# Kernel tuning notes

Measured on AMD Instinct MI355X. Metric: run time of the kernel, lower is better.

## Reference

```python
import jax, jax.numpy as jnp
import numpy as np

B, C, O, H, W = 8, 64, 64, 128, 128


def conv3x3(x, w, b):
    # x: [B,Cin,H,W], w: [Cout,Cin,3,3], stride 1, padding 1
    y = jax.lax.conv_general_dilated(
        x, w, window_strides=(1, 1), padding=((1, 1), (1, 1)),
        dimension_numbers=("NCHW", "OIHW", "NCHW"))
    return y + b[None, :, None, None]


def setup_inputs() -> dict:
    key = jax.random.key(0)
    ks = jax.random.split(key, 6)
    fan = C * 9
    x = jax.random.normal(ks[0], (B, C, H, W), dtype=jnp.float32)
    w_main = jax.random.normal(ks[1], (O, C, 3, 3), dtype=jnp.float32) / np.sqrt(fan)
    # small offset weights keep sampled locations near the regular grid (realistic post-training regime)
    w_offset = jax.random.normal(ks[2], (18, C, 3, 3), dtype=jnp.float32) * 0.05 / np.sqrt(fan)
    b_offset = jnp.zeros((18,), dtype=jnp.float32)
    w_mask = jax.random.normal(ks[3], (9, C, 3, 3), dtype=jnp.float32) / np.sqrt(fan)
    b_mask = jnp.zeros((9,), dtype=jnp.float32)
    return {"x": x, "w_main": w_main, "w_offset": w_offset,
            "b_offset": b_offset, "w_mask": w_mask, "b_mask": b_mask}


def deform_conv2d(x, w_main, offset, mask):
    # torchvision.ops.deform_conv2d: kernel 3x3, stride 1, pad 1, dilation 1, no bias
    Bb, Cc, Hh, Ww = x.shape
    Oo = w_main.shape[0]
    off = offset.reshape(Bb, 9, 2, Hh, Ww)
    dy, dx = off[:, :, 0], off[:, :, 1]            # [B,9,H,W]; pairs ordered (y,x), k row-major
    k = jnp.arange(9)
    kh = (k // 3 - 1).astype(x.dtype)              # kernel row offset in {-1,0,1}
    kw = (k % 3 - 1).astype(x.dtype)
    iy = jnp.arange(Hh, dtype=x.dtype)
    ix = jnp.arange(Ww, dtype=x.dtype)
    # sampling positions p = p0 + p_k + delta_p
    py = dy + iy[None, None, :, None] + kh[None, :, None, None]
    px = dx + ix[None, None, None, :] + kw[None, :, None, None]

    y0 = jnp.floor(py)
    x0 = jnp.floor(px)
    ly = py - y0
    lx = px - x0
    y0i = y0.astype(jnp.int32)
    x0i = x0.astype(jnp.int32)
    y1i = y0i + 1
    x1i = x0i + 1

    bidx = jnp.arange(Bb)[:, None, None, None]

    def corner(yi, xi, wgt):
        # zero-padding semantics: out-of-bounds neighbors contribute 0
        valid = (yi >= 0) & (yi < Hh) & (xi >= 0) & (xi < Ww)
        v = x[bidx, :, jnp.clip(yi, 0, Hh - 1), jnp.clip(xi, 0, Ww - 1)]  # [B,9,H,W,C]
        return v * (wgt * valid)[..., None]

    samp = (corner(y0i, x0i, (1 - ly) * (1 - lx))
            + corner(y0i, x1i, (1 - ly) * lx)
            + corner(y1i, x0i, ly * (1 - lx))
            + corner(y1i, x1i, ly * lx))
    samp = samp * mask[..., None]                  # modulation mask (dcn v2)
    # contract sampled patches with weights: [B,9,H,W,C] x [O,C,9] -> [B,O,H,W]
    return jnp.einsum("bkhwc,ock->bohw", samp, w_main.reshape(Oo, Cc, 9))


def reference(x, w_main, w_offset, b_offset, w_mask, b_mask):
    offset = conv3x3(x, w_offset, b_offset)                 # [B,18,H,W]
    mask = jax.nn.sigmoid(conv3x3(x, w_mask, b_mask))       # [B,9,H,W]
    return deform_conv2d(x, w_main, offset, mask)
```

## Files before the change

### kernel.cpp

```cpp
#include <hip/hip_runtime.h>
#include <math.h>

#define BB 8
#define CC 64
#define OO 64
#define HH 128
#define WW 128
#define HW (HH*WW)
#define NPIX (BB*HW)

typedef __bf16 bf16x8 __attribute__((ext_vector_type(8)));
typedef float floatx4 __attribute__((ext_vector_type(4)));
typedef float f32x2 __attribute__((ext_vector_type(2)));
typedef unsigned short ushort_t;

#define XT_BYTES  16777216
#define OM_BYTES  14680064
#define WT_BYTES  73728

__device__ __forceinline__ unsigned short f2b(float f) {
    unsigned u = __float_as_uint(f);
    u += 0x7fffu + ((u >> 16) & 1u);
    return (unsigned short)(u >> 16);
}

__device__ __forceinline__ unsigned cvt_pk_bf16(float lo, float hi) {
    unsigned r;
    asm("v_cvt_pk_bf16_f32 %0, %1, %2" : "=v"(r) : "v"(lo), "v"(hi));
    return r;
}

__device__ __forceinline__ f32x2 pk_fma(f32x2 a, f32x2 b, f32x2 c) {
    f32x2 d;
    asm("v_pk_fma_f32 %0, %1, %2, %3" : "=v"(d) : "v"(a), "v"(b), "v"(c));
    return d;
}

__device__ __forceinline__ f32x2 pk_mul(f32x2 a, f32x2 b) {
    f32x2 d;
    asm("v_pk_mul_f32 %0, %1, %2" : "=v"(d) : "v"(a), "v"(b));
    return d;
}

__global__ __launch_bounds__(256) void prep_kernel(
    const float* __restrict__ x,
    const float* __restrict__ wm, const float* __restrict__ woff,
    const float* __restrict__ wmask,
    ushort_t* __restrict__ xt, ushort_t* __restrict__ wt,
    ushort_t* __restrict__ wb)
{
    __shared__ float tile[64][33];
    int bid = blockIdx.x;
    int t   = threadIdx.x;

    if (bid < 4096) {
        int bh = bid >> 2;
        int w0 = (bid & 3) * 32;
        int b  = bh >> 7;
        int h  = bh & 127;
        int tx = t & 31;
        int ty = t >> 5;

        #pragma unroll
        for (int j = 0; j < 8; ++j) {
            int c = ty * 8 + j;
            tile[c][tx] = x[(((size_t)(b*CC + c))*HH + h)*WW + (w0 + tx)];
        }
        __syncthreads();
        #pragma unroll
        for (int j = 0; j < 4; ++j) {
            int w  = ty + 8*j;
            int cp = tx;
            unsigned u = cvt_pk_bf16(tile[2*cp][w], tile[2*cp+1][w]);
            *(unsigned*)(xt + (((size_t)(b*HH + h))*WW + (w0 + w))*CC + 2*cp) = u;
        }
    } else {
        int i = (bid - 4096) * 256 + t;
        if (i < 36864) {
            int o = i / 576, k = i % 576, tap = k >> 6, c = k & 63;
            wt[i] = f2b(wm[o*576 + c*9 + tap]);
        }
        int j = i - 36864;
        if (j >= 0 && j < 18432) {
            int o = j / 576, k = j % 576, tap = k >> 6, c = k & 63;
            float v = 0.f;
            if (o < 18)      v = woff[o*576 + c*9 + tap];
            else if (o < 27) v = wmask[(o-18)*576 + c*9 + tap];
            wb[j] = f2b(v);
        }
    }
}

#define SROW 200
#define WROW 72

__global__ __launch_bounds__(256, 4) void conv_deform_kernel(
    const ushort_t* __restrict__ xt, const ushort_t* __restrict__ wb,
    const float* __restrict__ boff, const float* __restrict__ bmsk,
    const ushort_t* __restrict__ wt, float* __restrict__ out)
{
    __shared__ ushort_t samp[64*SROW];
    __shared__ float om_lds[64][28];

    ushort_t* win = samp;

    int t = threadIdx.x;
    int lane = t & 63, wv = t >> 6;
    int bid = blockIdx.x;
    int b  = bid >> 8;
    int th = (bid >> 4) & 15;
    int tw = bid & 15;
    int h0 = th * 8, w0 = tw * 8;

    const ushort_t* xbase = xt + ((size_t)b << 20);
    int n = lane & 15, quad = lane >> 4;

    for (int idx = t; idx < 800; idx += 256) {
        int cell = idx >> 3;
        int ch   = (idx & 7) << 3;
        int cy = cell / 10, cx = cell - cy*10;
        int y = h0 + cy - 1, xx = w0 + cx - 1;
        uint4 val = make_uint4(0,0,0,0);
        if ((unsigned)y < (unsigned)HH && (unsigned)xx < (unsigned)WW)
            val = *(const uint4*)(xbase + (((y << 7) + xx) << 6) + ch);
        *(uint4*)(win + cell*WROW + ch) = val;
    }
    __syncthreads();

    {
        int p   = wv*16 + n;
        int cph = p >> 3, cpw = p & 7;
        const ushort_t* wb0 = wb + n*576;
        const ushort_t* wb1 = wb + (16 + n)*576;
        floatx4 c0 = (floatx4){0.f,0.f,0.f,0.f};
        floatx4 c1 = (floatx4){0.f,0.f,0.f,0.f};

        #pragma unroll
        for (int s = 0; s < 18; ++s) {
            int tap  = s >> 1;
            int tr   = tap / 3, tc = tap % 3;
            int coff = (s & 1)*32 + quad*8;
            bf16x8 b0 = *(const bf16x8*)(wb0 + tap*64 + coff);
            bf16x8 b1 = *(const bf16x8*)(wb1 + tap*64 + coff);
            bf16x8 a  = *(const bf16x8*)(win + ((cph + tr)*10 + (cpw + tc))*WROW + coff);
            c0 = __builtin_amdgcn_mfma_f32_16x16x32_bf16(a, b0, c0, 0, 0, 0);
            c1 = __builtin_amdgcn_mfma_f32_16x16x32_bf16(a, b1, c1, 0, 0, 0);
        }

        #pragma unroll
        for (int r = 0; r < 4; ++r) {
            int p_out = wv*16 + quad*4 + r;
            float* dst = &om_lds[p_out][0];
            dst[n] = c0[r] + boff[n];
            int o1 = 16 + n;
            if (o1 < 18) {
                dst[o1] = c1[r] + boff[o1];
            } else if (o1 < 27) {
                float z = c1[r] + bmsk[o1 - 18];
                dst[o1] = 1.f / (1.f + expf(-z));
            } else if (o1 == 27) {
                dst[27] = 0.f;
            }
        }
    }
    __syncthreads();

    int pa = t >> 2, cg = t & 3;
    int ph = pa >> 3, pw = pa & 7;
    int h_a = h0 + ph, w_a = w0 + pw;
    const float* omp = &om_lds[pa][0];

    floatx4 acc[4];
    #pragma unroll
    for (int i = 0; i < 4; ++i) acc[i] = (floatx4){0.f,0.f,0.f,0.f};
    const ushort_t* wrow = wt + (wv*16 + n)*576 + quad*8;

    float dyv[3], dxv[3], mv[3];
    #pragma unroll
    for (int j = 0; j < 3; ++j) {
        dyv[j] = omp[2*j]; dxv[j] = omp[2*j+1]; mv[j] = omp[18+j];
    }

    #pragma unroll
    for (int p = 0; p < 3; ++p) {
        bf16x8 wf[6];
        #pragma unroll
        for (int s = 0; s < 6; ++s)
            wf[s] = *(const bf16x8*)(wrow + (p*6 + s)*32);

        #pragma unroll
        for (int kk = 0; kk < 3; ++kk) {
            float py = (float)(h_a + p  - 1) + dyv[kk];
            float px = (float)(w_a + kk - 1) + dxv[kk];
            float y0f = floorf(py), x0f = floorf(px);
            float ly = py - y0f, lx = px - x0f;
            int y0 = (int)y0f, x0 = (int)x0f, y1 = y0 + 1, x1 = x0 + 1;
            float vy0 = ((unsigned)y0 < (unsigned)HH) ? 1.f : 0.f;
            float vy1 = ((unsigned)y1 < (unsigned)HH) ? 1.f : 0.f;
            float vx0 = ((unsigned)x0 < (unsigned)WW) ? 1.f : 0.f;
            float vx1 = ((unsigned)x1 < (unsigned)WW) ? 1.f : 0.f;
            float m   = mv[kk];

            float cw[4] = { (1.f-ly)*(1.f-lx)*vy0*vx0*m,
                            (1.f-ly)*lx      *vy0*vx1*m,
                            ly*(1.f-lx)      *vy1*vx0*m,
                            ly*lx            *vy1*vx1*m };
            int ys[4] = { y0, y0, y1, y1 };
            int xs[4] = { x0, x1, x0, x1 };

            uint4 q[8];
            #pragma unroll
            for (int cn = 0; cn < 4; ++cn) {
                int yc = min(max(ys[cn], 0), HH-1);
                int xc = min(max(xs[cn], 0), WW-1);
                const uint4* cp = (const uint4*)(xbase + (((yc << 7) + xc) << 6) + cg*16);
                q[2*cn]   = cp[0];
                q[2*cn+1] = cp[1];
            }

            f32x2 v2[8];
            {
                f32x2 w2; w2.x = cw[0]; w2.y = cw[0];
                unsigned u0[8] = { q[0].x, q[0].y, q[0].z, q[0].w,
                                   q[1].x, q[1].y, q[1].z, q[1].w };
                #pragma unroll
                for (int j = 0; j < 8; ++j) {
                    f32x2 f;
                    f.x = __uint_as_float(u0[j] << 16);
                    f.y = __uint_as_float(u0[j] & 0xffff0000u);
                    v2[j] = pk_mul(f, w2);
                }
            }
            #pragma unroll
            for (int cn = 1; cn < 4; ++cn) {
                f32x2 w2; w2.x = cw[cn]; w2.y = cw[cn];
                unsigned u0[8] = { q[2*cn].x, q[2*cn].y, q[2*cn].z, q[2*cn].w,
                                   q[2*cn+1].x, q[2*cn+1].y, q[2*cn+1].z, q[2*cn+1].w };
                #pragma unroll
                for (int j = 0; j < 8; ++j) {
                    f32x2 f;
                    f.x = __uint_as_float(u0[j] << 16);
                    f.y = __uint_as_float(u0[j] & 0xffff0000u);
                    v2[j] = pk_fma(f, w2, v2[j]);
                }
            }

            {
                unsigned uu[8];
                #pragma unroll
                for (int j = 0; j < 8; ++j)
                    uu[j] = cvt_pk_bf16(v2[j].x, v2[j].y);
                uint4* dst = (uint4*)(samp + pa*SROW + kk*64 + cg*16);
                dst[0] = make_uint4(uu[0], uu[1], uu[2], uu[3]);
                dst[1] = make_uint4(uu[4], uu[5], uu[6], uu[7]);
            }
        }

        float dyn_[3], dxn_[3], mn_[3];
        if (p < 2) {
            #pragma unroll
            for (int j = 0; j < 3; ++j) {
                int k2 = 3*(p+1) + j;
                dyn_[j] = omp[2*k2]; dxn_[j] = omp[2*k2+1]; mn_[j] = omp[18+k2];
            }
        }

        __syncthreads();

        #pragma unroll
        for (int kk = 0; kk < 3; ++kk) {
            #pragma unroll
            for (int half = 0; half < 2; ++half) {
                bf16x8 bfrag = wf[kk*2 + half];
                #pragma unroll
                for (int mt = 0; mt < 4; ++mt) {
                    bf16x8 afrag = *(const bf16x8*)(samp + (mt*16 + n)*SROW
                                                    + kk*64 + half*32 + quad*8);
                    acc[mt] = __builtin_amdgcn_mfma_f32_16x16x32_bf16(
                                  afrag, bfrag, acc[mt], 0, 0, 0);
                }
            }
        }

        if (p < 2) {
            __syncthreads();
            #pragma unroll
            for (int j = 0; j < 3; ++j) {
                dyv[j] = dyn_[j]; dxv[j] = dxn_[j]; mv[j] = mn_[j];
            }
        }
    }

    float* op = out + ((size_t)b*OO + (wv*16 + n))*HW;
    #pragma unroll
    for (int mt = 0; mt < 4; ++mt) {
        int row = h0 + mt*2 + (quad >> 1);
        int col = w0 + (quad & 1)*4;
        float4 st = make_float4(acc[mt][0], acc[mt][1], acc[mt][2], acc[mt][3]);
        *(float4*)(op + row*WW + col) = st;
    }
}

extern "C" void kernel_launch(void* const* d_in, const int* in_sizes, int n_in,
                              void* d_out, int out_size, void* d_ws, size_t ws_size,
                              hipStream_t stream)
{
    const float* x      = (const float*)d_in[0];
    const float* w_main = (const float*)d_in[1];
    const float* w_off  = (const float*)d_in[2];
    const float* b_off  = (const float*)d_in[3];
    const float* w_msk  = (const float*)d_in[4];
    const float* b_msk  = (const float*)d_in[5];
    float* out = (float*)d_out;

    unsigned char* ws = (unsigned char*)d_ws;
    ushort_t* xt = (ushort_t*)ws;
    ushort_t* wt = (ushort_t*)(ws + XT_BYTES + OM_BYTES);
    ushort_t* wb = (ushort_t*)(ws + XT_BYTES + OM_BYTES + WT_BYTES);

    prep_kernel<<<4096 + 216, 256, 0, stream>>>(x, w_main, w_off, w_msk, xt, wt, wb);

    conv_deform_kernel<<<NPIX/64, 256, 0, stream>>>(xt, wb, b_off, b_msk, wt, out);
}
```

Measured before the change: 164.7 us.

## Serve bilinear samples from a widened LDS halo, vectorize prep loads

The conv stage's input window grows from a 10x10 to a 12x12 halo in its own LDS buffer. The deformable sampling stage reads its four bilinear corners from this halo whenever every lane's nonzero-weight corners fall inside it, and falls back to global loads otherwise. This targets the global/L2 gather traffic, relying on offsets staying small. The prep kernel's x transpose now uses float4 loads. In exchange, LDS use rises and occupancy drops from 4 to 3 blocks, and a wave-wide vote adds a branch.

```diff
diff --git a/kernel.cpp b/kernel.cpp
--- a/kernel.cpp
+++ b/kernel.cpp
@@ -58,15 +58,22 @@
         int w0 = (bid & 3) * 32;
         int b  = bh >> 7;
         int h  = bh & 127;
+
+        {
+            int c  = t >> 2;
+            int wq = t & 3;
+            const float* src = x + (((size_t)(b*CC + c))*HH + h)*WW + (w0 + wq*8);
+            float4 v0 = ((const float4*)src)[0];
+            float4 v1 = ((const float4*)src)[1];
+            int wbse = wq*8;
+            tile[c][wbse+0] = v0.x; tile[c][wbse+1] = v0.y;
+            tile[c][wbse+2] = v0.z; tile[c][wbse+3] = v0.w;
+            tile[c][wbse+4] = v1.x; tile[c][wbse+5] = v1.y;
+            tile[c][wbse+6] = v1.z; tile[c][wbse+7] = v1.w;
+        }
+        __syncthreads();
         int tx = t & 31;
         int ty = t >> 5;
-
-        #pragma unroll
-        for (int j = 0; j < 8; ++j) {
-            int c = ty * 8 + j;
-            tile[c][tx] = x[(((size_t)(b*CC + c))*HH + h)*WW + (w0 + tx)];
-        }
-        __syncthreads();
         #pragma unroll
         for (int j = 0; j < 4; ++j) {
             int w  = ty + 8*j;
@@ -94,15 +101,14 @@
 #define SROW 200
 #define WROW 72
 
-__global__ __launch_bounds__(256, 4) void conv_deform_kernel(
+__global__ __launch_bounds__(256, 3) void conv_deform_kernel(
     const ushort_t* __restrict__ xt, const ushort_t* __restrict__ wb,
     const float* __restrict__ boff, const float* __restrict__ bmsk,
     const ushort_t* __restrict__ wt, float* __restrict__ out)
 {
+    __shared__ ushort_t halo[144*WROW];
     __shared__ ushort_t samp[64*SROW];
     __shared__ float om_lds[64][28];
-
-    ushort_t* win = samp;
 
     int t = threadIdx.x;
     int lane = t & 63, wv = t >> 6;
@@ -115,15 +121,15 @@
     const ushort_t* xbase = xt + ((size_t)b << 20);
     int n = lane & 15, quad = lane >> 4;
 
-    for (int idx = t; idx < 800; idx += 256) {
+    for (int idx = t; idx < 1152; idx += 256) {
         int cell = idx >> 3;
         int ch   = (idx & 7) << 3;
-        int cy = cell / 10, cx = cell - cy*10;
-        int y = h0 + cy - 1, xx = w0 + cx - 1;
+        int cy = cell / 12, cx = cell - cy*12;
+        int y = h0 + cy - 2, xx = w0 + cx - 2;
         uint4 val = make_uint4(0,0,0,0);
         if ((unsigned)y < (unsigned)HH && (unsigned)xx < (unsigned)WW)
             val = *(const uint4*)(xbase + (((y << 7) + xx) << 6) + ch);
-        *(uint4*)(win + cell*WROW + ch) = val;
+        *(uint4*)(halo + cell*WROW + ch) = val;
     }
     __syncthreads();
 
@@ -142,7 +148,7 @@
             int coff = (s & 1)*32 + quad*8;
             bf16x8 b0 = *(const bf16x8*)(wb0 + tap*64 + coff);
             bf16x8 b1 = *(const bf16x8*)(wb1 + tap*64 + coff);
-            bf16x8 a  = *(const bf16x8*)(win + ((cph + tr)*10 + (cpw + tc))*WROW + coff);
+            bf16x8 a  = *(const bf16x8*)(halo + ((cph + tr + 1)*12 + (cpw + tc + 1))*WROW + coff);
             c0 = __builtin_amdgcn_mfma_f32_16x16x32_bf16(a, b0, c0, 0, 0, 0);
             c1 = __builtin_amdgcn_mfma_f32_16x16x32_bf16(a, b1, c1, 0, 0, 0);
         }
@@ -208,14 +214,34 @@
             int ys[4] = { y0, y0, y1, y1 };
             int xs[4] = { x0, x1, x0, x1 };
 
-            uint4 q[8];
+            int ycl[4], xcl[4], hidx[4];
+            int ok = 1;
             #pragma unroll
             for (int cn = 0; cn < 4; ++cn) {
                 int yc = min(max(ys[cn], 0), HH-1);
                 int xc = min(max(xs[cn], 0), WW-1);
-                const uint4* cp = (const uint4*)(xbase + (((yc << 7) + xc) << 6) + cg*16);
-                q[2*cn]   = cp[0];
-                q[2*cn+1] = cp[1];
+                ycl[cn] = yc; xcl[cn] = xc;
+                int hy = yc - h0 + 2, hx = xc - w0 + 2;
+                int inh = ((unsigned)hy < 12u) & ((unsigned)hx < 12u);
+                ok &= ((cw[cn] == 0.f) | inh);
+                hidx[cn] = min(max(hy, 0), 11)*12 + min(max(hx, 0), 11);
+            }
+
+            uint4 q[8];
+            if (__all(ok)) {
+                #pragma unroll
+                for (int cn = 0; cn < 4; ++cn) {
+                    const uint4* cp = (const uint4*)(halo + hidx[cn]*WROW + cg*16);
+                    q[2*cn]   = cp[0];
+                    q[2*cn+1] = cp[1];
+                }
+            } else {
+                #pragma unroll
+                for (int cn = 0; cn < 4; ++cn) {
+                    const uint4* cp = (const uint4*)(xbase + (((ycl[cn] << 7) + xcl[cn]) << 6) + cg*16);
+                    q[2*cn]   = cp[0];
+                    q[2*cn+1] = cp[1];
+                }
             }
 
             f32x2 v2[8];
```

After: 163.7 us. Within noise of the previous version (-0.6%).
